# Kernel optimization log

Measured on AMD Instinct MI355X. Metric: run time of the kernel, lower is better.

Reference implementation:

```python
import jax, jax.numpy as jnp
import numpy as np

D_MODEL = 1024
N_HEADS = 16
HEAD_DIM = D_MODEL // N_HEADS
SPARSITY = 0.5  # torch.rand(...) < sparsity_factor -> True means masked (disallowed)


def setup_inputs() -> dict:
    key = jax.random.key(0)
    ks = jax.random.split(key, 12)
    B, S, D = 2, 2048, D_MODEL
    query = jax.random.normal(ks[0], (B, S, D), dtype=jnp.float32)
    key_t = jax.random.normal(ks[1], (B, S, D), dtype=jnp.float32)
    value = jax.random.normal(ks[2], (B, S, D), dtype=jnp.float32)
    # per-forward random boolean mask, materialized deterministically here
    mask = jax.random.uniform(ks[3], (B, S, S)) < SPARSITY
    scale = 1.0 / np.sqrt(D)
    Wq = jax.random.uniform(ks[4], (D, D), jnp.float32, -scale, scale)
    Wk = jax.random.uniform(ks[5], (D, D), jnp.float32, -scale, scale)
    Wv = jax.random.uniform(ks[6], (D, D), jnp.float32, -scale, scale)
    Wo = jax.random.uniform(ks[7], (D, D), jnp.float32, -scale, scale)
    bq = jnp.zeros((D,), jnp.float32)
    bk = jnp.zeros((D,), jnp.float32)
    bv = jnp.zeros((D,), jnp.float32)
    bo = jnp.zeros((D,), jnp.float32)
    return {"query": query, "key": key_t, "value": value, "mask": mask,
            "Wq": Wq, "Wk": Wk, "Wv": Wv, "Wo": Wo,
            "bq": bq, "bk": bk, "bv": bv, "bo": bo}


def reference(query, key, value, mask, Wq, Wk, Wv, Wo, bq, bk, bv, bo):
    B, S, D = query.shape
    H, hd = N_HEADS, HEAD_DIM
    # in-projections (torch uses x @ W.T + b)
    q = (query @ Wq.T + bq).reshape(B, S, H, hd).transpose(0, 2, 1, 3)  # (B,H,S,hd)
    k = (key @ Wk.T + bk).reshape(B, S, H, hd).transpose(0, 2, 1, 3)
    v = (value @ Wv.T + bv).reshape(B, S, H, hd).transpose(0, 2, 1, 3)
    scores = jnp.einsum('bhqd,bhkd->bhqk', q, k) / jnp.sqrt(jnp.float32(hd))
    # bool mask: True = disallowed; broadcast over heads
    scores = jnp.where(mask[:, None, :, :], -jnp.inf, scores)
    attn = jax.nn.softmax(scores, axis=-1)  # dropout inactive at eval
    out = jnp.einsum('bhqk,bhkd->bhqd', attn, v)  # (B,H,S,hd)
    out = out.transpose(0, 2, 1, 3).reshape(B, S, D)
    return out @ Wo.T + bo
```

## Files before the change

### kernel.cpp

```cpp
#include <hip/hip_runtime.h>
#include <stdint.h>

#define MTOK   4096
#define DMODEL 1024
#define SEQ    2048
#define NH     16
#define HD     64
#define LDK    72
#define LDP    72
#define QSCL   0.18033688f
#define NWORDS (2 * SEQ * SEQ / 64)

typedef _Float16 h8  __attribute__((ext_vector_type(8)));
typedef _Float16 h4  __attribute__((ext_vector_type(4)));
typedef _Float16 h2  __attribute__((ext_vector_type(2)));
typedef __fp16   fp16x2 __attribute__((ext_vector_type(2)));
typedef float    f16v __attribute__((ext_vector_type(16)));
typedef float    f4  __attribute__((ext_vector_type(4)));

typedef __attribute__((address_space(1))) const unsigned int g_u32;
typedef __attribute__((address_space(3))) unsigned int       l_u32;

__device__ __forceinline__ void g2l16(const void* g, void* l) {
    __builtin_amdgcn_global_load_lds((g_u32*)(unsigned long long)g,
                                     (l_u32*)(unsigned int)(unsigned long long)l,
                                     16, 0, 0);
}

__device__ __forceinline__ h2 pkrtz(float a, float b) {
    fp16x2 r = __builtin_amdgcn_cvt_pkrtz(a, b);
    return __builtin_bit_cast(h2, r);
}

#if __has_builtin(__builtin_amdgcn_exp2f)
#define E2(x) __builtin_amdgcn_exp2f(x)
#else
#define E2(x) exp2f(x)
#endif

__global__ void detect_mask_kernel(const unsigned char* __restrict__ m,
                                   int* __restrict__ flag) {
    int t = threadIdx.x;
    int cnt = 0;
    for (int i = 0; i < 128; ++i)
        cnt += (m[t * 128 + i] != 0) ? 1 : 0;
#pragma unroll
    for (int off = 32; off > 0; off >>= 1)
        cnt += __shfl_down(cnt, off, 64);
    if (t == 0) *flag = (cnt > 2500) ? 1 : 0;
}

__global__ __launch_bounds__(256) void prep_kernel(
    const float* __restrict__ s0, const float* __restrict__ s1,
    const float* __restrict__ s2, const float* __restrict__ s3,
    const float* __restrict__ s4, const float* __restrict__ s5,
    const float* __restrict__ s6,
    _Float16* __restrict__ d0, _Float16* __restrict__ d1,
    _Float16* __restrict__ d2, _Float16* __restrict__ d3,
    _Float16* __restrict__ d4, _Float16* __restrict__ d5,
    _Float16* __restrict__ d6,
    const unsigned char* __restrict__ mb, const unsigned int* __restrict__ mu,
    const int* __restrict__ flagp, unsigned long long* __restrict__ mout) {
    const int z = blockIdx.y;
    const int gid = blockIdx.x * 256 + threadIdx.x;
    const int stride = gridDim.x * 256;
    if (z < 7) {
        const float* s = (z == 0) ? s0 : (z == 1) ? s1 : (z == 2) ? s2
                       : (z == 3) ? s3 : (z == 4) ? s4 : (z == 5) ? s5 : s6;
        _Float16* d = (z == 0) ? d0 : (z == 1) ? d1 : (z == 2) ? d2
                    : (z == 3) ? d3 : (z == 4) ? d4 : (z == 5) ? d5 : d6;
        const int n4 = (z < 3) ? (MTOK * DMODEL / 4) : (DMODEL * DMODEL / 4);
        for (int i = gid; i < n4; i += stride) {
            float4 v = ((const float4*)s)[i];
            h4 o = {(_Float16)v.x, (_Float16)v.y, (_Float16)v.z, (_Float16)v.w};
            ((h4*)d)[i] = o;
        }
    } else {
        const int byteflag = *flagp;
        for (int w = gid; w < NWORDS; w += stride) {
            unsigned long long bits = 0ull;
            if (byteflag) {
                const uint4* p = (const uint4*)(mb + (size_t)w * 64);
#pragma unroll
                for (int i = 0; i < 4; ++i) {
                    uint4 v = p[i];
                    unsigned dw[4] = {v.x, v.y, v.z, v.w};
#pragma unroll
                    for (int j = 0; j < 4; ++j) {
                        unsigned d = dw[j];
                        unsigned nib = (unsigned)((d & 0xFFu) != 0)
                                     | ((unsigned)((d & 0xFF00u) != 0) << 1)
                                     | ((unsigned)((d & 0xFF0000u) != 0) << 2)
                                     | ((unsigned)((d >> 24) != 0) << 3);
                        bits |= (unsigned long long)nib << (i * 16 + j * 4);
                    }
                }
            } else {
                const uint4* p = (const uint4*)(mu + (size_t)w * 64);
#pragma unroll
                for (int i = 0; i < 16; ++i) {
                    uint4 v = p[i];
                    unsigned nib = (unsigned)(v.x != 0u)
                                 | ((unsigned)(v.y != 0u) << 1)
                                 | ((unsigned)(v.z != 0u) << 2)
                                 | ((unsigned)(v.w != 0u) << 3);
                    bits |= (unsigned long long)nib << (i * 4);
                }
            }
            mout[w] = bits;
        }
    }
}

template <int MODE>
__device__ __forceinline__ void gemm16_body(const _Float16* __restrict__ A,
                                            const _Float16* __restrict__ W,
                                            const float* __restrict__ bias,
                                            void* __restrict__ outv,
                                            float scale) {
    __shared__ __align__(16) _Float16 Asb[128 * 32];
    __shared__ __align__(16) _Float16 Bsb[128 * 32];
    const int tid = threadIdx.x;
    const int wv = tid >> 6, lane = tid & 63;
    const int l15 = lane & 15, g = lane >> 4;
    const int wy = wv >> 1, wx = wv & 1;
    const int m0 = blockIdx.x * 128, n0 = blockIdx.y * 128;

    f4 acc[4][4];
#pragma unroll
    for (int i = 0; i < 4; ++i)
#pragma unroll
        for (int j = 0; j < 4; ++j) acc[i][j] = (f4){0.f, 0.f, 0.f, 0.f};

    const int o0 = tid * 16;
    const int o1 = (256 + tid) * 16;
    const int r0 = o0 >> 6, c0b = o0 & 63;
    const int r1 = o1 >> 6, c1b = o1 & 63;
    const char* Ab = (const char*)A;
    const char* Wb = (const char*)W;

    for (int kt = 0; kt < 32; ++kt) {
        const int k0b = kt * 64;
        __syncthreads();
        g2l16(Ab + (size_t)(m0 + r0) * 2048 + k0b + c0b, (char*)Asb + o0);
        g2l16(Ab + (size_t)(m0 + r1) * 2048 + k0b + c1b, (char*)Asb + o1);
        g2l16(Wb + (size_t)(n0 + r0) * 2048 + k0b + c0b, (char*)Bsb + o0);
        g2l16(Wb + (size_t)(n0 + r1) * 2048 + k0b + c1b, (char*)Bsb + o1);
        __syncthreads();

        h8 af[4], bf[4];
#pragma unroll
        for (int t = 0; t < 4; ++t) {
            af[t] = *(const h8*)(Asb + (wy * 64 + t * 16 + l15) * 32 + g * 8);
            bf[t] = *(const h8*)(Bsb + (wx * 64 + t * 16 + l15) * 32 + g * 8);
        }
#pragma unroll
        for (int i = 0; i < 4; ++i)
#pragma unroll
            for (int j = 0; j < 4; ++j) {
                if (MODE == 2)
                    acc[i][j] = __builtin_amdgcn_mfma_f32_16x16x32_f16(
                        bf[j], af[i], acc[i][j], 0, 0, 0);
                else
                    acc[i][j] = __builtin_amdgcn_mfma_f32_16x16x32_f16(
                        af[i], bf[j], acc[i][j], 0, 0, 0);
            }
    }

#pragma unroll
    for (int j = 0; j < 4; ++j) {
#pragma unroll
        for (int i = 0; i < 4; ++i) {
            if (MODE == 2) {
                const int m = m0 + wy * 64 + i * 16 + l15;
                const int b = m >> 11, s = m & 2047;
#pragma unroll
                for (int r = 0; r < 4; ++r) {
                    const int n = n0 + wx * 64 + j * 16 + g * 4 + r;
                    const int h = n >> 6, d = n & 63;
                    ((_Float16*)outv)[(((size_t)(b * NH + h)) * HD + d) * SEQ + s] =
                        (_Float16)(acc[i][j][r] + bias[n]);
                }
            } else {
                const int n = n0 + wx * 64 + j * 16 + l15;
                const float bb = bias[n];
                const int mbase = m0 + wy * 64 + i * 16 + g * 4;
                if (MODE == 1) {
                    const int h = n >> 6, d = n & 63;
#pragma unroll
                    for (int r = 0; r < 4; ++r) {
                        const int m = mbase + r;
                        const int b = m >> 11, s = m & 2047;
                        ((_Float16*)outv)[(((size_t)(b * NH + h)) * SEQ + s) * HD + d] =
                            (_Float16)((acc[i][j][r] + bb) * scale);
                    }
                } else {
#pragma unroll
                    for (int r = 0; r < 4; ++r)
                        ((float*)outv)[(size_t)(mbase + r) * DMODEL + n] =
                            acc[i][j][r] + bb;
                }
            }
        }
    }
}

__global__ __launch_bounds__(256) void qkv_gemm16_kernel(
    const _Float16* __restrict__ xq, const _Float16* __restrict__ xk,
    const _Float16* __restrict__ xv,
    const _Float16* __restrict__ Wq, const _Float16* __restrict__ Wk,
    const _Float16* __restrict__ Wv,
    const float* __restrict__ bq, const float* __restrict__ bk,
    const float* __restrict__ bv,
    _Float16* __restrict__ q_out, _Float16* __restrict__ k_out,
    _Float16* __restrict__ vt_out) {
    const int z = blockIdx.z;
    if (z == 0)      gemm16_body<1>(xq, Wq, bq, (void*)q_out, QSCL);
    else if (z == 1) gemm16_body<1>(xk, Wk, bk, (void*)k_out, 1.0f);
    else             gemm16_body<2>(xv, Wv, bv, (void*)vt_out, 1.0f);
}

__global__ __launch_bounds__(256) void out_gemm16_kernel(
    const _Float16* __restrict__ X, const _Float16* __restrict__ W,
    const float* __restrict__ bias, float* __restrict__ out) {
    gemm16_body<0>(X, W, bias, (void*)out, 1.0f);
}

__global__ __launch_bounds__(256) void attn_kernel(
    const _Float16* __restrict__ Q, const _Float16* __restrict__ K,
    const _Float16* __restrict__ Vt,
    const unsigned long long* __restrict__ mbits,
    _Float16* __restrict__ out) {
    __shared__ __align__(16) _Float16 Ks[2][64 * LDK];
    __shared__ __align__(16) _Float16 Vs[2][64 * LDK];
    __shared__ __align__(16) _Float16 Ps[128 * LDP];

    const int tid = threadIdx.x;
    const int wv = tid >> 6, lane = tid & 63;
    const int l31 = lane & 31, hi = lane >> 5;
    const int q0 = blockIdx.x * 128;
    const int bh = blockIdx.y;
    const int b = bh >> 4, h = bh & 15;
    const size_t bho = (size_t)bh * (SEQ * HD);
    const int qrow = q0 + wv * 32 + l31;

    h8 qf[4];
    const _Float16* qp = Q + bho + (size_t)qrow * HD;
#pragma unroll
    for (int ks = 0; ks < 4; ++ks) qf[ks] = *(const h8*)(qp + ks * 16 + hi * 8);

    f16v Ot[2];
#pragma unroll
    for (int mt = 0; mt < 2; ++mt)
#pragma unroll
        for (int r = 0; r < 16; ++r) Ot[mt][r] = 0.f;
    float l_r = 0.f;

    const int sr = tid >> 2;
    const int scol = (tid & 3) * 16;
    const _Float16* kg = K + bho;
    const _Float16* vg = Vt + bho;
    _Float16* prow = &Ps[(wv * 32 + l31) * LDP];
    const unsigned long long* mrow =
        mbits + ((size_t)b * SEQ + qrow) * (SEQ / 64);

    h8 kr0 = *(const h8*)(kg + (size_t)sr * HD + scol);
    h8 kr1 = *(const h8*)(kg + (size_t)sr * HD + scol + 8);
    h8 vr0 = *(const h8*)(vg + (size_t)sr * SEQ + scol);
    h8 vr1 = *(const h8*)(vg + (size_t)sr * SEQ + scol + 8);
    uint2 mw = *(const uint2*)(mrow);
    *(h8*)(&Ks[0][sr * LDK + scol])     = kr0;
    *(h8*)(&Ks[0][sr * LDK + scol + 8]) = kr1;
    *(h8*)(&Vs[0][sr * LDK + scol])     = vr0;
    *(h8*)(&Vs[0][sr * LDK + scol + 8]) = vr1;
    __syncthreads();

    for (int kt = 0; kt < 32; ++kt) {
        const int cur = kt & 1;
        uint2 mw_n;
        if (kt < 31) {
            const int k0n = (kt + 1) * 64;
            kr0 = *(const h8*)(kg + (size_t)(k0n + sr) * HD + scol);
            kr1 = *(const h8*)(kg + (size_t)(k0n + sr) * HD + scol + 8);
            vr0 = *(const h8*)(vg + (size_t)sr * SEQ + k0n + scol);
            vr1 = *(const h8*)(vg + (size_t)sr * SEQ + k0n + scol + 8);
            mw_n = *(const uint2*)(mrow + kt + 1);
        }

        f16v sc0, sc1;
#pragma unroll
        for (int r = 0; r < 16; ++r) { sc0[r] = 0.f; sc1[r] = 0.f; }
#pragma unroll
        for (int ks = 0; ks < 4; ++ks) {
            h8 kf0 = *(const h8*)(&Ks[cur][l31 * LDK + ks * 16 + hi * 8]);
            h8 kf1 = *(const h8*)(&Ks[cur][(32 + l31) * LDK + ks * 16 + hi * 8]);
            sc0 = __builtin_amdgcn_mfma_f32_32x32x16_f16(kf0, qf[ks], sc0, 0, 0, 0);
            sc1 = __builtin_amdgcn_mfma_f32_32x32x16_f16(kf1, qf[ks], sc1, 0, 0, 0);
        }

        float ps = 0.f;
#pragma unroll
        for (int mt = 0; mt < 2; ++mt) {
            const unsigned w = mt ? mw.y : mw.x;
            const f16v& s = mt ? sc1 : sc0;
#pragma unroll
            for (int g4 = 0; g4 < 4; ++g4) {
                const int sh = g4 * 8 + hi * 4;
                float p0 = E2(((w >> (sh + 0)) & 1u) ? -1e30f : s[g4 * 4 + 0]);
                float p1 = E2(((w >> (sh + 1)) & 1u) ? -1e30f : s[g4 * 4 + 1]);
                float p2 = E2(((w >> (sh + 2)) & 1u) ? -1e30f : s[g4 * 4 + 2]);
                float p3 = E2(((w >> (sh + 3)) & 1u) ? -1e30f : s[g4 * 4 + 3]);
                h2 lo  = pkrtz(p0, p1);
                h2 hi2 = pkrtz(p2, p3);
                ps += p0 + p1 + p2 + p3;
                h4 ph = {lo.x, lo.y, hi2.x, hi2.y};
                *(h4*)(prow + mt * 32 + g4 * 8 + hi * 4) = ph;
            }
        }
        l_r += ps;

        h8 pf[4];
#pragma unroll
        for (int ks = 0; ks < 4; ++ks)
            pf[ks] = *(const h8*)(prow + ks * 16 + hi * 8);
#pragma unroll
        for (int ks = 0; ks < 4; ++ks) {
            h8 vf0 = *(const h8*)(&Vs[cur][l31 * LDK + ks * 16 + hi * 8]);
            h8 vf1 = *(const h8*)(&Vs[cur][(32 + l31) * LDK + ks * 16 + hi * 8]);
            Ot[0] = __builtin_amdgcn_mfma_f32_32x32x16_f16(vf0, pf[ks], Ot[0], 0, 0, 0);
            Ot[1] = __builtin_amdgcn_mfma_f32_32x32x16_f16(vf1, pf[ks], Ot[1], 0, 0, 0);
        }

        if (kt < 31) {
            const int nxt = cur ^ 1;
            *(h8*)(&Ks[nxt][sr * LDK + scol])     = kr0;
            *(h8*)(&Ks[nxt][sr * LDK + scol + 8]) = kr1;
            *(h8*)(&Vs[nxt][sr * LDK + scol])     = vr0;
            *(h8*)(&Vs[nxt][sr * LDK + scol + 8]) = vr1;
            mw = mw_n;
        }
        __syncthreads();
    }

    l_r += __shfl_xor(l_r, 32);
    const float inv = 1.0f / l_r;
    _Float16* op = out + ((size_t)b * SEQ + qrow) * DMODEL + h * HD;
#pragma unroll
    for (int mt = 0; mt < 2; ++mt)
#pragma unroll
        for (int g4 = 0; g4 < 4; ++g4) {
            const int d = mt * 32 + g4 * 8 + hi * 4;
            h4 ov = {(_Float16)(Ot[mt][g4 * 4 + 0] * inv),
                     (_Float16)(Ot[mt][g4 * 4 + 1] * inv),
                     (_Float16)(Ot[mt][g4 * 4 + 2] * inv),
                     (_Float16)(Ot[mt][g4 * 4 + 3] * inv)};
            *(h4*)(op + d) = ov;
        }
}

extern "C" void kernel_launch(void* const* d_in, const int* in_sizes, int n_in,
                              void* d_out, int out_size, void* d_ws, size_t ws_size,
                              hipStream_t stream) {
    const float* query = (const float*)d_in[0];
    const float* key_  = (const float*)d_in[1];
    const float* value = (const float*)d_in[2];
    const void*  mask  = d_in[3];
    const float* Wq = (const float*)d_in[4];
    const float* Wk = (const float*)d_in[5];
    const float* Wv = (const float*)d_in[6];
    const float* Wo = (const float*)d_in[7];
    const float* bq = (const float*)d_in[8];
    const float* bk = (const float*)d_in[9];
    const float* bv = (const float*)d_in[10];
    const float* bo = (const float*)d_in[11];

    char* ws = (char*)d_ws;
    int* flag = (int*)ws;
    _Float16* xq  = (_Float16*)(ws + 256);
    _Float16* xk  = xq + (size_t)MTOK * DMODEL;
    _Float16* xv  = xk + (size_t)MTOK * DMODEL;
    _Float16* Wqh = xv + (size_t)MTOK * DMODEL;
    _Float16* Wkh = Wqh + (size_t)DMODEL * DMODEL;
    _Float16* Wvh = Wkh + (size_t)DMODEL * DMODEL;
    _Float16* Woh = Wvh + (size_t)DMODEL * DMODEL;
    _Float16* q_ws  = Woh + (size_t)DMODEL * DMODEL;
    _Float16* k_ws  = q_ws + (size_t)MTOK * DMODEL;
    _Float16* vt_ws = k_ws + (size_t)MTOK * DMODEL;
    _Float16* a_ws  = vt_ws + (size_t)MTOK * DMODEL;
    unsigned long long* mb_ws =
        (unsigned long long*)(a_ws + (size_t)MTOK * DMODEL);

    detect_mask_kernel<<<1, 64, 0, stream>>>((const unsigned char*)mask, flag);

    prep_kernel<<<dim3(1024, 8), 256, 0, stream>>>(
        query, key_, value, Wq, Wk, Wv, Wo, xq, xk, xv, Wqh, Wkh, Wvh, Woh,
        (const unsigned char*)mask, (const unsigned int*)mask, flag, mb_ws);

    dim3 gqkv(MTOK / 128, DMODEL / 128, 3);
    qkv_gemm16_kernel<<<gqkv, 256, 0, stream>>>(xq, xk, xv, Wqh, Wkh, Wvh,
                                                bq, bk, bv, q_ws, k_ws, vt_ws);

    dim3 gattn(SEQ / 128, 2 * NH);
    attn_kernel<<<gattn, 256, 0, stream>>>(q_ws, k_ws, vt_ws, mb_ws, a_ws);

    dim3 gout(MTOK / 128, DMODEL / 128);
    out_gemm16_kernel<<<gout, 256, 0, stream>>>(a_ws, Woh, bo, (float*)d_out);
}
```

Baseline: 284.3 us.

## Fold mask-format detection into prep, shuffle P via registers, retile output GEMM

Removes the separate single-block mask detection kernel; each mask block of the prep kernel now counts nonzero bytes itself and reduces the count through shared memory. In attention, the softmax probabilities are passed to the PV MFMA by cross-lane shuffles instead of a round trip through an LDS P buffer, which drops that shared memory and adds an occupancy hint of 4. The output projection GEMM uses 64-wide N tiles, doubling its block count for better CU fill. The costs are a redundant mask scan in every mask block, extra shuffle and select instructions, and lower per-block reuse in the output GEMM.

```diff
diff --git a/kernel.cpp b/kernel.cpp
--- a/kernel.cpp
+++ b/kernel.cpp
@@ -7,7 +7,6 @@
 #define NH     16
 #define HD     64
 #define LDK    72
-#define LDP    72
 #define QSCL   0.18033688f
 #define NWORDS (2 * SEQ * SEQ / 64)
 
@@ -27,9 +26,9 @@
                                      16, 0, 0);
 }
 
-__device__ __forceinline__ h2 pkrtz(float a, float b) {
+__device__ __forceinline__ unsigned pkrtz_u(float a, float b) {
     fp16x2 r = __builtin_amdgcn_cvt_pkrtz(a, b);
-    return __builtin_bit_cast(h2, r);
+    return __builtin_bit_cast(unsigned, r);
 }
 
 #if __has_builtin(__builtin_amdgcn_exp2f)
@@ -37,18 +36,6 @@
 #else
 #define E2(x) exp2f(x)
 #endif
-
-__global__ void detect_mask_kernel(const unsigned char* __restrict__ m,
-                                   int* __restrict__ flag) {
-    int t = threadIdx.x;
-    int cnt = 0;
-    for (int i = 0; i < 128; ++i)
-        cnt += (m[t * 128 + i] != 0) ? 1 : 0;
-#pragma unroll
-    for (int off = 32; off > 0; off >>= 1)
-        cnt += __shfl_down(cnt, off, 64);
-    if (t == 0) *flag = (cnt > 2500) ? 1 : 0;
-}
 
 __global__ __launch_bounds__(256) void prep_kernel(
     const float* __restrict__ s0, const float* __restrict__ s1,
@@ -60,7 +47,7 @@
     _Float16* __restrict__ d4, _Float16* __restrict__ d5,
     _Float16* __restrict__ d6,
     const unsigned char* __restrict__ mb, const unsigned int* __restrict__ mu,
-    const int* __restrict__ flagp, unsigned long long* __restrict__ mout) {
+    unsigned long long* __restrict__ mout) {
     const int z = blockIdx.y;
     const int gid = blockIdx.x * 256 + threadIdx.x;
     const int stride = gridDim.x * 256;
@@ -76,7 +63,20 @@
             ((h4*)d)[i] = o;
         }
     } else {
-        const int byteflag = *flagp;
+        __shared__ int wsum[4];
+        int cnt = 0;
+        const uchar4* mp4 = (const uchar4*)mb;
+#pragma unroll
+        for (int i = 0; i < 8; ++i) {
+            uchar4 v = mp4[threadIdx.x * 8 + i];
+            cnt += (v.x != 0) + (v.y != 0) + (v.z != 0) + (v.w != 0);
+        }
+#pragma unroll
+        for (int off = 32; off > 0; off >>= 1) cnt += __shfl_down(cnt, off, 64);
+        if ((threadIdx.x & 63) == 0) wsum[threadIdx.x >> 6] = cnt;
+        __syncthreads();
+        const int byteflag = (wsum[0] + wsum[1] + wsum[2] + wsum[3]) > 2500;
+
         for (int w = gid; w < NWORDS; w += stride) {
             unsigned long long bits = 0ull;
             if (byteflag) {
@@ -112,52 +112,54 @@
     }
 }
 
-template <int MODE>
+template <int MODE, int BN>
 __device__ __forceinline__ void gemm16_body(const _Float16* __restrict__ A,
                                             const _Float16* __restrict__ W,
                                             const float* __restrict__ bias,
                                             void* __restrict__ outv,
                                             float scale) {
     __shared__ __align__(16) _Float16 Asb[128 * 32];
-    __shared__ __align__(16) _Float16 Bsb[128 * 32];
+    __shared__ __align__(16) _Float16 Bsb[BN * 32];
+    constexpr int NJ = BN / 32;
     const int tid = threadIdx.x;
     const int wv = tid >> 6, lane = tid & 63;
     const int l15 = lane & 15, g = lane >> 4;
     const int wy = wv >> 1, wx = wv & 1;
-    const int m0 = blockIdx.x * 128, n0 = blockIdx.y * 128;
-
-    f4 acc[4][4];
+    const int m0 = blockIdx.x * 128, n0 = blockIdx.y * BN;
+
+    f4 acc[4][NJ];
 #pragma unroll
     for (int i = 0; i < 4; ++i)
 #pragma unroll
-        for (int j = 0; j < 4; ++j) acc[i][j] = (f4){0.f, 0.f, 0.f, 0.f};
-
-    const int o0 = tid * 16;
-    const int o1 = (256 + tid) * 16;
-    const int r0 = o0 >> 6, c0b = o0 & 63;
-    const int r1 = o1 >> 6, c1b = o1 & 63;
+        for (int j = 0; j < NJ; ++j) acc[i][j] = (f4){0.f, 0.f, 0.f, 0.f};
+
+    const int oA0 = tid * 16, oA1 = (256 + tid) * 16;
+    const int rA0 = oA0 >> 6, cA0 = oA0 & 63;
+    const int rA1 = oA1 >> 6, cA1 = oA1 & 63;
     const char* Ab = (const char*)A;
     const char* Wb = (const char*)W;
 
     for (int kt = 0; kt < 32; ++kt) {
         const int k0b = kt * 64;
         __syncthreads();
-        g2l16(Ab + (size_t)(m0 + r0) * 2048 + k0b + c0b, (char*)Asb + o0);
-        g2l16(Ab + (size_t)(m0 + r1) * 2048 + k0b + c1b, (char*)Asb + o1);
-        g2l16(Wb + (size_t)(n0 + r0) * 2048 + k0b + c0b, (char*)Bsb + o0);
-        g2l16(Wb + (size_t)(n0 + r1) * 2048 + k0b + c1b, (char*)Bsb + o1);
+        g2l16(Ab + (size_t)(m0 + rA0) * 2048 + k0b + cA0, (char*)Asb + oA0);
+        g2l16(Ab + (size_t)(m0 + rA1) * 2048 + k0b + cA1, (char*)Asb + oA1);
+        g2l16(Wb + (size_t)(n0 + rA0) * 2048 + k0b + cA0, (char*)Bsb + oA0);
+        if (BN == 128)
+            g2l16(Wb + (size_t)(n0 + rA1) * 2048 + k0b + cA1, (char*)Bsb + oA1);
         __syncthreads();
 
-        h8 af[4], bf[4];
-#pragma unroll
-        for (int t = 0; t < 4; ++t) {
+        h8 af[4], bf[NJ];
+#pragma unroll
+        for (int t = 0; t < 4; ++t)
             af[t] = *(const h8*)(Asb + (wy * 64 + t * 16 + l15) * 32 + g * 8);
-            bf[t] = *(const h8*)(Bsb + (wx * 64 + t * 16 + l15) * 32 + g * 8);
-        }
+#pragma unroll
+        for (int t = 0; t < NJ; ++t)
+            bf[t] = *(const h8*)(Bsb + (wx * (BN / 2) + t * 16 + l15) * 32 + g * 8);
 #pragma unroll
         for (int i = 0; i < 4; ++i)
 #pragma unroll
-            for (int j = 0; j < 4; ++j) {
+            for (int j = 0; j < NJ; ++j) {
                 if (MODE == 2)
                     acc[i][j] = __builtin_amdgcn_mfma_f32_16x16x32_f16(
                         bf[j], af[i], acc[i][j], 0, 0, 0);
@@ -168,7 +170,7 @@
     }
 
 #pragma unroll
-    for (int j = 0; j < 4; ++j) {
+    for (int j = 0; j < NJ; ++j) {
 #pragma unroll
         for (int i = 0; i < 4; ++i) {
             if (MODE == 2) {
@@ -176,13 +178,13 @@
                 const int b = m >> 11, s = m & 2047;
 #pragma unroll
                 for (int r = 0; r < 4; ++r) {
-                    const int n = n0 + wx * 64 + j * 16 + g * 4 + r;
+                    const int n = n0 + wx * (BN / 2) + j * 16 + g * 4 + r;
                     const int h = n >> 6, d = n & 63;
                     ((_Float16*)outv)[(((size_t)(b * NH + h)) * HD + d) * SEQ + s] =
                         (_Float16)(acc[i][j][r] + bias[n]);
                 }
             } else {
-                const int n = n0 + wx * 64 + j * 16 + l15;
+                const int n = n0 + wx * (BN / 2) + j * 16 + l15;
                 const float bb = bias[n];
                 const int mbase = m0 + wy * 64 + i * 16 + g * 4;
                 if (MODE == 1) {
@@ -215,25 +217,24 @@
     _Float16* __restrict__ q_out, _Float16* __restrict__ k_out,
     _Float16* __restrict__ vt_out) {
     const int z = blockIdx.z;
-    if (z == 0)      gemm16_body<1>(xq, Wq, bq, (void*)q_out, QSCL);
-    else if (z == 1) gemm16_body<1>(xk, Wk, bk, (void*)k_out, 1.0f);
-    else             gemm16_body<2>(xv, Wv, bv, (void*)vt_out, 1.0f);
+    if (z == 0)      gemm16_body<1, 128>(xq, Wq, bq, (void*)q_out, QSCL);
+    else if (z == 1) gemm16_body<1, 128>(xk, Wk, bk, (void*)k_out, 1.0f);
+    else             gemm16_body<2, 128>(xv, Wv, bv, (void*)vt_out, 1.0f);
 }
 
 __global__ __launch_bounds__(256) void out_gemm16_kernel(
     const _Float16* __restrict__ X, const _Float16* __restrict__ W,
     const float* __restrict__ bias, float* __restrict__ out) {
-    gemm16_body<0>(X, W, bias, (void*)out, 1.0f);
-}
-
-__global__ __launch_bounds__(256) void attn_kernel(
+    gemm16_body<0, 64>(X, W, bias, (void*)out, 1.0f);
+}
+
+__global__ __launch_bounds__(256, 4) void attn_kernel(
     const _Float16* __restrict__ Q, const _Float16* __restrict__ K,
     const _Float16* __restrict__ Vt,
     const unsigned long long* __restrict__ mbits,
     _Float16* __restrict__ out) {
     __shared__ __align__(16) _Float16 Ks[2][64 * LDK];
     __shared__ __align__(16) _Float16 Vs[2][64 * LDK];
-    __shared__ __align__(16) _Float16 Ps[128 * LDP];
 
     const int tid = threadIdx.x;
     const int wv = tid >> 6, lane = tid & 63;
@@ -260,7 +261,6 @@
     const int scol = (tid & 3) * 16;
     const _Float16* kg = K + bho;
     const _Float16* vg = Vt + bho;
-    _Float16* prow = &Ps[(wv * 32 + l31) * LDP];
     const unsigned long long* mrow =
         mbits + ((size_t)b * SEQ + qrow) * (SEQ / 64);
 
@@ -299,6 +299,7 @@
         }
 
         float ps = 0.f;
+        unsigned Du[2][4][2];
 #pragma unroll
         for (int mt = 0; mt < 2; ++mt) {
             const unsigned w = mt ? mw.y : mw.x;
@@ -310,19 +311,33 @@
                 float p1 = E2(((w >> (sh + 1)) & 1u) ? -1e30f : s[g4 * 4 + 1]);
                 float p2 = E2(((w >> (sh + 2)) & 1u) ? -1e30f : s[g4 * 4 + 2]);
                 float p3 = E2(((w >> (sh + 3)) & 1u) ? -1e30f : s[g4 * 4 + 3]);
-                h2 lo  = pkrtz(p0, p1);
-                h2 hi2 = pkrtz(p2, p3);
+                Du[mt][g4][0] = pkrtz_u(p0, p1);
+                Du[mt][g4][1] = pkrtz_u(p2, p3);
                 ps += p0 + p1 + p2 + p3;
-                h4 ph = {lo.x, lo.y, hi2.x, hi2.y};
-                *(h4*)(prow + mt * 32 + g4 * 8 + hi * 4) = ph;
             }
         }
         l_r += ps;
 
         h8 pf[4];
 #pragma unroll
-        for (int ks = 0; ks < 4; ++ks)
-            pf[ks] = *(const h8*)(prow + ks * 16 + hi * 8);
+        for (int ks = 0; ks < 4; ++ks) {
+            const int mtc = ks >> 1, base = (ks & 1) * 2;
+            const unsigned A0 = Du[mtc][base][0],     A1 = Du[mtc][base][1];
+            const unsigned B0 = Du[mtc][base + 1][0], B1 = Du[mtc][base + 1][1];
+            const unsigned s0 = hi ? A0 : B0;
+            const unsigned s1 = hi ? A1 : B1;
+            const unsigned o0 = hi ? B0 : A0;
+            const unsigned o1 = hi ? B1 : A1;
+            const unsigned r0 = (unsigned)__shfl_xor((int)s0, 32, 64);
+            const unsigned r1 = (unsigned)__shfl_xor((int)s1, 32, 64);
+            uint4 fv;
+            fv.x = hi ? r0 : o0;
+            fv.y = hi ? r1 : o1;
+            fv.z = hi ? o0 : r0;
+            fv.w = hi ? o1 : r1;
+            pf[ks] = __builtin_bit_cast(h8, fv);
+        }
+
 #pragma unroll
         for (int ks = 0; ks < 4; ++ks) {
             h8 vf0 = *(const h8*)(&Vs[cur][l31 * LDK + ks * 16 + hi * 8]);
@@ -375,7 +390,6 @@
     const float* bo = (const float*)d_in[11];
 
     char* ws = (char*)d_ws;
-    int* flag = (int*)ws;
     _Float16* xq  = (_Float16*)(ws + 256);
     _Float16* xk  = xq + (size_t)MTOK * DMODEL;
     _Float16* xv  = xk + (size_t)MTOK * DMODEL;
@@ -390,11 +404,9 @@
     unsigned long long* mb_ws =
         (unsigned long long*)(a_ws + (size_t)MTOK * DMODEL);
 
-    detect_mask_kernel<<<1, 64, 0, stream>>>((const unsigned char*)mask, flag);
-
     prep_kernel<<<dim3(1024, 8), 256, 0, stream>>>(
         query, key_, value, Wq, Wk, Wv, Wo, xq, xk, xv, Wqh, Wkh, Wvh, Woh,
-        (const unsigned char*)mask, (const unsigned int*)mask, flag, mb_ws);
+        (const unsigned char*)mask, (const unsigned int*)mask, mb_ws);
 
     dim3 gqkv(MTOK / 128, DMODEL / 128, 3);
     qkv_gemm16_kernel<<<gqkv, 256, 0, stream>>>(xq, xk, xv, Wqh, Wkh, Wvh,
@@ -403,6 +415,6 @@
     dim3 gattn(SEQ / 128, 2 * NH);
     attn_kernel<<<gattn, 256, 0, stream>>>(q_ws, k_ws, vt_ws, mb_ws, a_ws);
 
-    dim3 gout(MTOK / 128, DMODEL / 128);
+    dim3 gout(MTOK / 128, DMODEL / 64);
     out_gemm16_kernel<<<gout, 256, 0, stream>>>(a_ws, Woh, bo, (float*)d_out);
 }
```

New measurement: 282.7 us. About the same (-0.5%).

## Deepen GEMM K-tile with XOR-swizzled LDS, smaller out tile, fold mask detect

Applied to the files above, without the earlier changes.

The GEMM body now loads a 128-wide K slice per iteration (16 iterations instead of 32), which halves the barrier count. It stores tiles in LDS with an XOR swizzle to avoid bank conflicts on fragment reads. The output projection uses 64x128 tiles to double the block count and improve occupancy and CU coverage. The separate mask-format detection kernel is removed, and each mask-conversion block now computes the flag itself. That drops one launch but makes every such block redo the small sampling reduction.

```diff
diff --git a/kernel.cpp b/kernel.cpp
--- a/kernel.cpp
+++ b/kernel.cpp
@@ -37,18 +37,6 @@
 #else
 #define E2(x) exp2f(x)
 #endif
-
-__global__ void detect_mask_kernel(const unsigned char* __restrict__ m,
-                                   int* __restrict__ flag) {
-    int t = threadIdx.x;
-    int cnt = 0;
-    for (int i = 0; i < 128; ++i)
-        cnt += (m[t * 128 + i] != 0) ? 1 : 0;
-#pragma unroll
-    for (int off = 32; off > 0; off >>= 1)
-        cnt += __shfl_down(cnt, off, 64);
-    if (t == 0) *flag = (cnt > 2500) ? 1 : 0;
-}
 
 __global__ __launch_bounds__(256) void prep_kernel(
     const float* __restrict__ s0, const float* __restrict__ s1,
@@ -60,7 +48,7 @@
     _Float16* __restrict__ d4, _Float16* __restrict__ d5,
     _Float16* __restrict__ d6,
     const unsigned char* __restrict__ mb, const unsigned int* __restrict__ mu,
-    const int* __restrict__ flagp, unsigned long long* __restrict__ mout) {
+    unsigned long long* __restrict__ mout) {
     const int z = blockIdx.y;
     const int gid = blockIdx.x * 256 + threadIdx.x;
     const int stride = gridDim.x * 256;
@@ -76,7 +64,20 @@
             ((h4*)d)[i] = o;
         }
     } else {
-        const int byteflag = *flagp;
+        __shared__ int wsum[4];
+        int cnt = 0;
+        const uchar4* mp4 = (const uchar4*)mb;
+#pragma unroll
+        for (int i = 0; i < 8; ++i) {
+            uchar4 v = mp4[threadIdx.x * 8 + i];
+            cnt += (v.x != 0) + (v.y != 0) + (v.z != 0) + (v.w != 0);
+        }
+#pragma unroll
+        for (int off = 32; off > 0; off >>= 1) cnt += __shfl_down(cnt, off, 64);
+        if ((threadIdx.x & 63) == 0) wsum[threadIdx.x >> 6] = cnt;
+        __syncthreads();
+        const int byteflag = (wsum[0] + wsum[1] + wsum[2] + wsum[3]) > 2500;
+
         for (int w = gid; w < NWORDS; w += stride) {
             unsigned long long bits = 0ull;
             if (byteflag) {
@@ -112,79 +113,107 @@
     }
 }
 
-template <int MODE>
+template <int MODE, int BM, int BN>
 __device__ __forceinline__ void gemm16_body(const _Float16* __restrict__ A,
                                             const _Float16* __restrict__ W,
                                             const float* __restrict__ bias,
                                             void* __restrict__ outv,
                                             float scale) {
-    __shared__ __align__(16) _Float16 Asb[128 * 32];
-    __shared__ __align__(16) _Float16 Bsb[128 * 32];
+    __shared__ __align__(16) _Float16 Asb[BM * 64];
+    __shared__ __align__(16) _Float16 Bsb[BN * 64];
+    constexpr int NI = BM / 32, NJ = BN / 32;
+    constexpr int WM = BM / 2,  WN = BN / 2;
+    constexpr int RA = BM * 128 / 4096;
+    constexpr int RB = BN * 128 / 4096;
     const int tid = threadIdx.x;
     const int wv = tid >> 6, lane = tid & 63;
     const int l15 = lane & 15, g = lane >> 4;
     const int wy = wv >> 1, wx = wv & 1;
-    const int m0 = blockIdx.x * 128, n0 = blockIdx.y * 128;
-
-    f4 acc[4][4];
-#pragma unroll
-    for (int i = 0; i < 4; ++i)
-#pragma unroll
-        for (int j = 0; j < 4; ++j) acc[i][j] = (f4){0.f, 0.f, 0.f, 0.f};
-
-    const int o0 = tid * 16;
-    const int o1 = (256 + tid) * 16;
-    const int r0 = o0 >> 6, c0b = o0 & 63;
-    const int r1 = o1 >> 6, c1b = o1 & 63;
+    const int m0 = blockIdx.x * BM, n0 = blockIdx.y * BN;
+
+    f4 acc[NI][NJ];
+#pragma unroll
+    for (int i = 0; i < NI; ++i)
+#pragma unroll
+        for (int j = 0; j < NJ; ++j) acc[i][j] = (f4){0.f, 0.f, 0.f, 0.f};
+
     const char* Ab = (const char*)A;
     const char* Wb = (const char*)W;
-
-    for (int kt = 0; kt < 32; ++kt) {
-        const int k0b = kt * 64;
+    int srowA[RA], scolA[RA];
+#pragma unroll
+    for (int r = 0; r < RA; ++r) {
+        const int o = (r * 256 + tid) * 16;
+        srowA[r] = o >> 7;
+        scolA[r] = (((o >> 4) & 7) ^ (srowA[r] & 7)) * 16;
+    }
+    int srowB[RB], scolB[RB];
+#pragma unroll
+    for (int r = 0; r < RB; ++r) {
+        const int o = (r * 256 + tid) * 16;
+        srowB[r] = o >> 7;
+        scolB[r] = (((o >> 4) & 7) ^ (srowB[r] & 7)) * 16;
+    }
+
+    for (int kt = 0; kt < 16; ++kt) {
+        const int k0b = kt * 128;
         __syncthreads();
-        g2l16(Ab + (size_t)(m0 + r0) * 2048 + k0b + c0b, (char*)Asb + o0);
-        g2l16(Ab + (size_t)(m0 + r1) * 2048 + k0b + c1b, (char*)Asb + o1);
-        g2l16(Wb + (size_t)(n0 + r0) * 2048 + k0b + c0b, (char*)Bsb + o0);
-        g2l16(Wb + (size_t)(n0 + r1) * 2048 + k0b + c1b, (char*)Bsb + o1);
+#pragma unroll
+        for (int r = 0; r < RA; ++r)
+            g2l16(Ab + (size_t)(m0 + srowA[r]) * 2048 + k0b + scolA[r],
+                  (char*)Asb + (r * 256 + tid) * 16);
+#pragma unroll
+        for (int r = 0; r < RB; ++r)
+            g2l16(Wb + (size_t)(n0 + srowB[r]) * 2048 + k0b + scolB[r],
+                  (char*)Bsb + (r * 256 + tid) * 16);
         __syncthreads();
 
-        h8 af[4], bf[4];
-#pragma unroll
-        for (int t = 0; t < 4; ++t) {
-            af[t] = *(const h8*)(Asb + (wy * 64 + t * 16 + l15) * 32 + g * 8);
-            bf[t] = *(const h8*)(Bsb + (wx * 64 + t * 16 + l15) * 32 + g * 8);
-        }
-#pragma unroll
-        for (int i = 0; i < 4; ++i)
-#pragma unroll
-            for (int j = 0; j < 4; ++j) {
-                if (MODE == 2)
-                    acc[i][j] = __builtin_amdgcn_mfma_f32_16x16x32_f16(
-                        bf[j], af[i], acc[i][j], 0, 0, 0);
-                else
-                    acc[i][j] = __builtin_amdgcn_mfma_f32_16x16x32_f16(
-                        af[i], bf[j], acc[i][j], 0, 0, 0);
+#pragma unroll
+        for (int ksub = 0; ksub < 2; ++ksub) {
+            h8 af[NI], bf[NJ];
+#pragma unroll
+            for (int t = 0; t < NI; ++t) {
+                const int row = wy * WM + t * 16 + l15;
+                const int pos = (ksub * 4 + g) ^ (row & 7);
+                af[t] = *(const h8*)(Asb + row * 64 + pos * 8);
             }
-    }
-
-#pragma unroll
-    for (int j = 0; j < 4; ++j) {
-#pragma unroll
-        for (int i = 0; i < 4; ++i) {
+#pragma unroll
+            for (int t = 0; t < NJ; ++t) {
+                const int row = wx * WN + t * 16 + l15;
+                const int pos = (ksub * 4 + g) ^ (row & 7);
+                bf[t] = *(const h8*)(Bsb + row * 64 + pos * 8);
+            }
+#pragma unroll
+            for (int i = 0; i < NI; ++i)
+#pragma unroll
+                for (int j = 0; j < NJ; ++j) {
+                    if (MODE == 2)
+                        acc[i][j] = __builtin_amdgcn_mfma_f32_16x16x32_f16(
+                            bf[j], af[i], acc[i][j], 0, 0, 0);
+                    else
+                        acc[i][j] = __builtin_amdgcn_mfma_f32_16x16x32_f16(
+                            af[i], bf[j], acc[i][j], 0, 0, 0);
+                }
+        }
+    }
+
+#pragma unroll
+    for (int j = 0; j < NJ; ++j) {
+#pragma unroll
+        for (int i = 0; i < NI; ++i) {
             if (MODE == 2) {
-                const int m = m0 + wy * 64 + i * 16 + l15;
+                const int m = m0 + wy * WM + i * 16 + l15;
                 const int b = m >> 11, s = m & 2047;
 #pragma unroll
                 for (int r = 0; r < 4; ++r) {
-                    const int n = n0 + wx * 64 + j * 16 + g * 4 + r;
+                    const int n = n0 + wx * WN + j * 16 + g * 4 + r;
                     const int h = n >> 6, d = n & 63;
                     ((_Float16*)outv)[(((size_t)(b * NH + h)) * HD + d) * SEQ + s] =
                         (_Float16)(acc[i][j][r] + bias[n]);
                 }
             } else {
-                const int n = n0 + wx * 64 + j * 16 + l15;
+                const int n = n0 + wx * WN + j * 16 + l15;
                 const float bb = bias[n];
-                const int mbase = m0 + wy * 64 + i * 16 + g * 4;
+                const int mbase = m0 + wy * WM + i * 16 + g * 4;
                 if (MODE == 1) {
                     const int h = n >> 6, d = n & 63;
 #pragma unroll
@@ -215,15 +244,15 @@
     _Float16* __restrict__ q_out, _Float16* __restrict__ k_out,
     _Float16* __restrict__ vt_out) {
     const int z = blockIdx.z;
-    if (z == 0)      gemm16_body<1>(xq, Wq, bq, (void*)q_out, QSCL);
-    else if (z == 1) gemm16_body<1>(xk, Wk, bk, (void*)k_out, 1.0f);
-    else             gemm16_body<2>(xv, Wv, bv, (void*)vt_out, 1.0f);
+    if (z == 0)      gemm16_body<1, 128, 128>(xq, Wq, bq, (void*)q_out, QSCL);
+    else if (z == 1) gemm16_body<1, 128, 128>(xk, Wk, bk, (void*)k_out, 1.0f);
+    else             gemm16_body<2, 128, 128>(xv, Wv, bv, (void*)vt_out, 1.0f);
 }
 
 __global__ __launch_bounds__(256) void out_gemm16_kernel(
     const _Float16* __restrict__ X, const _Float16* __restrict__ W,
     const float* __restrict__ bias, float* __restrict__ out) {
-    gemm16_body<0>(X, W, bias, (void*)out, 1.0f);
+    gemm16_body<0, 64, 128>(X, W, bias, (void*)out, 1.0f);
 }
 
 __global__ __launch_bounds__(256) void attn_kernel(
@@ -375,7 +404,6 @@
     const float* bo = (const float*)d_in[11];
 
     char* ws = (char*)d_ws;
-    int* flag = (int*)ws;
     _Float16* xq  = (_Float16*)(ws + 256);
     _Float16* xk  = xq + (size_t)MTOK * DMODEL;
     _Float16* xv  = xk + (size_t)MTOK * DMODEL;
@@ -390,11 +418,9 @@
     unsigned long long* mb_ws =
         (unsigned long long*)(a_ws + (size_t)MTOK * DMODEL);
 
-    detect_mask_kernel<<<1, 64, 0, stream>>>((const unsigned char*)mask, flag);
-
     prep_kernel<<<dim3(1024, 8), 256, 0, stream>>>(
         query, key_, value, Wq, Wk, Wv, Wo, xq, xk, xv, Wqh, Wkh, Wvh, Woh,
-        (const unsigned char*)mask, (const unsigned int*)mask, flag, mb_ws);
+        (const unsigned char*)mask, (const unsigned int*)mask, mb_ws);
 
     dim3 gqkv(MTOK / 128, DMODEL / 128, 3);
     qkv_gemm16_kernel<<<gqkv, 256, 0, stream>>>(xq, xk, xv, Wqh, Wkh, Wvh,
@@ -403,6 +429,6 @@
     dim3 gattn(SEQ / 128, 2 * NH);
     attn_kernel<<<gattn, 256, 0, stream>>>(q_ws, k_ws, vt_ws, mb_ws, a_ws);
 
-    dim3 gout(MTOK / 128, DMODEL / 128);
+    dim3 gout(MTOK / 64, DMODEL / 128);
     out_gemm16_kernel<<<gout, 256, 0, stream>>>(a_ws, Woh, bo, (float*)d_out);
 }
```

Measured after the change: 270.3 us. 1.05x faster.
